# Performance work log

Measured on AMD Instinct MI355X. Metric: run time of the kernel, lower is better.

Reference implementation:

```python
import jax, jax.numpy as jnp
import numpy as np

FEAT_STRIDE = 16
SCALES = np.array([4.0, 8.0, 16.0])
RATIOS = np.array([0.5, 1.0, 2.0])
SAMPLE_DURATION = 16
TIME_DIM = [16]
NUM_ANCHORS = 9
BATCH = 32
FEAT_H = 64
FEAT_W = 64
POST_NMS_TOPN = 300


def _whctrs(a):
    w = a[2] - a[0] + 1.0
    h = a[3] - a[1] + 1.0
    return w, h, a[0] + 0.5 * (w - 1.0), a[1] + 0.5 * (h - 1.0)


def _mkanchors(ws, hs, xc, yc):
    ws = ws[:, None]
    hs = hs[:, None]
    return np.hstack([xc - 0.5 * (ws - 1.0), yc - 0.5 * (hs - 1.0),
                      xc + 0.5 * (ws - 1.0), yc + 0.5 * (hs - 1.0)])


def _generate_anchors(base_size=16, ratios=RATIOS, scales=SCALES):
    base = np.array([1.0, 1.0, base_size, base_size]) - 1.0
    w, h, xc, yc = _whctrs(base)
    size = w * h
    ws = np.round(np.sqrt(size / ratios))
    hs = np.round(ws * ratios)
    ratio_anchors = _mkanchors(ws, hs, xc, yc)
    out = []
    for i in range(ratio_anchors.shape[0]):
        w_i, h_i, x_i, y_i = _whctrs(ratio_anchors[i])
        out.append(_mkanchors(w_i * scales, h_i * scales, x_i, y_i))
    return np.vstack(out).astype(np.float32)  # (A, 4)


def _anchors_all(feat_h, feat_w):
    # shifted anchors over the feature grid, then temporal tiling per time_dim
    anchors = _generate_anchors()                                  # (A, 4)
    sx = np.arange(feat_w) * FEAT_STRIDE
    sy = np.arange(feat_h) * FEAT_STRIDE
    mx, my = np.meshgrid(sx, sy)
    shifts = np.stack([mx.ravel(), my.ravel(), mx.ravel(), my.ravel()], 1).astype(np.float32)
    anc = (anchors[None, :, :] + shifts[:, None, :]).reshape(-1, 4)  # (K*A, 4)
    sd = SAMPLE_DURATION
    parts = []
    for t in TIME_DIM:
        for j in range(sd - t + 1):
            full = np.zeros((sd, anc.shape[0], 4), np.float32)
            full[j:j + t] = anc
            parts.append(full.transpose(1, 0, 2))                   # (K*A, sd, 4)
    return np.concatenate(parts, 0).reshape(-1, sd * 4)             # (N, sd*4)


def setup_inputs() -> dict:
    key = jax.random.key(0)
    k1, k2 = jax.random.split(key)
    scores_in = jax.random.normal(k1, (BATCH, 2 * NUM_ANCHORS, FEAT_H, FEAT_W), jnp.float32)
    bbox_frame = jax.random.normal(k2, (BATCH, NUM_ANCHORS * SAMPLE_DURATION * 4, FEAT_H, FEAT_W), jnp.float32)
    im_info = jnp.tile(jnp.array([[FEAT_H * 16.0, FEAT_W * 16.0, 1.0]], jnp.float32), (BATCH, 1))
    return {"scores_in": scores_in, "bbox_frame": bbox_frame, "im_info": im_info,
            "post_nms_topN": POST_NMS_TOPN}


def reference(scores_in, bbox_frame, im_info, post_nms_topN):
    B, _, H, W = scores_in.shape
    sd4 = SAMPLE_DURATION * 4
    # fg scores -> (B, K*A) in (h, w, a) order matching the anchor layout
    scores = scores_in[:, NUM_ANCHORS:].transpose(0, 2, 3, 1).reshape(B, -1)
    deltas = bbox_frame.transpose(0, 2, 3, 1).reshape(B, -1, sd4)
    aa = jnp.asarray(_anchors_all(H, W))                             # (N, sd*4)
    # bbox_transform_inv with weights (1,1,1,1), per-frame groups of 4
    bb = aa.reshape(1, -1, SAMPLE_DURATION, 4)                       # (1, N, sd, 4)
    dd = deltas.reshape(B, -1, SAMPLE_DURATION, 4)                   # (B, N, sd, 4)
    w = bb[..., 2] - bb[..., 0] + 1.0
    h = bb[..., 3] - bb[..., 1] + 1.0
    cx = bb[..., 0] + 0.5 * w
    cy = bb[..., 1] + 0.5 * h
    pcx = dd[..., 0] * w + cx
    pcy = dd[..., 1] * h + cy
    pw = jnp.exp(dd[..., 2]) * w
    ph = jnp.exp(dd[..., 3]) * h
    # clip to image bounds per batch element
    xmax = im_info[:, 1, None, None] - 1.0                           # (B,1,1)
    ymax = im_info[:, 0, None, None] - 1.0
    x1 = jnp.clip(pcx - 0.5 * pw, 0.0, xmax)
    y1 = jnp.clip(pcy - 0.5 * ph, 0.0, ymax)
    x2 = jnp.clip(pcx + 0.5 * pw, 0.0, xmax)
    y2 = jnp.clip(pcy + 0.5 * ph, 0.0, ymax)
    proposals = jnp.stack([x1, y1, x2, y2], -1).reshape(B, -1, sd4)  # (B, N, sd*4)
    # per-image descending sort + top-k gather (the torch code applies no real NMS)
    top_scores, top_idx = jax.lax.top_k(scores, post_nms_topN)       # (B, topN)
    top_props = jnp.take_along_axis(proposals, top_idx[:, :, None], axis=1)
    batch_col = jnp.broadcast_to(jnp.arange(B, dtype=proposals.dtype)[:, None],
                                 (B, post_nms_topN))
    out = jnp.concatenate([batch_col[..., None], top_props, top_scores[..., None]], -1)
    return out  # (B, post_nms_topN, sd*4 + 2)
```

## Files before the change

kernel.cpp:

```cpp
#include <hip/hip_runtime.h>
#include <math.h>

#define BATCH    32
#define FH       64
#define FW       64
#define NA       9
#define NSCORE   (FH*FW*NA)
#define TOPN     300
#define SD       16
#define NTHREADS 1024
#define NBINS    16384
#define NWORDS   (NBINS/2)
#define CAND_CAP 1024

__constant__ float c_aw[NA] = {92.f,184.f,368.f,64.f,128.f,256.f,44.f,88.f,176.f};
__constant__ float c_ah[NA] = {48.f,96.f,192.f,64.f,128.f,256.f,88.f,176.f,352.f};

__device__ __forceinline__ unsigned f2key(float f) {
    unsigned u = __float_as_uint(f);
    return (u & 0x80000000u) ? ~u : (u | 0x80000000u);
}
__device__ __forceinline__ float key2f(unsigned k) {
    unsigned u = (k & 0x80000000u) ? (k & 0x7FFFFFFFu) : ~k;
    return __uint_as_float(u);
}

__global__ __launch_bounds__(NTHREADS)
void proposal_topk_kernel(const float* __restrict__ scores_in,
                          const float* __restrict__ bbox,
                          const float* __restrict__ im_info,
                          float* __restrict__ out)
{
    const int b   = blockIdx.x;
    const int tid = threadIdx.x;
    const float* sc = scores_in + ((size_t)b * 18 + NA) * (FH * FW);
    const float4* sc4 = (const float4*)sc;

    __shared__ unsigned hist[NWORDS];
    __shared__ unsigned pscan[NTHREADS];
    __shared__ unsigned long long cand[CAND_CAP];
    __shared__ unsigned s_t14, s_nsel;

    for (int i = tid; i < NWORDS; i += NTHREADS) hist[i] = 0u;
    __syncthreads();
    for (int j = tid; j < NSCORE / 4; j += NTHREADS) {
        float4 v = sc4[j];
        unsigned d0 = f2key(v.x) >> 18;
        unsigned d1 = f2key(v.y) >> 18;
        unsigned d2 = f2key(v.z) >> 18;
        unsigned d3 = f2key(v.w) >> 18;
        atomicAdd(&hist[d0 >> 1], 1u << ((d0 & 1u) << 4));
        atomicAdd(&hist[d1 >> 1], 1u << ((d1 & 1u) << 4));
        atomicAdd(&hist[d2 >> 1], 1u << ((d2 & 1u) << 4));
        atomicAdd(&hist[d3 >> 1], 1u << ((d3 & 1u) << 4));
    }
    __syncthreads();

    unsigned w[8];
    unsigned local = 0u;
    #pragma unroll
    for (int i = 0; i < 8; ++i) {
        w[i] = hist[tid * 8 + i];
        local += (w[i] & 0xFFFFu) + (w[i] >> 16);
    }
    pscan[tid] = local;
    __syncthreads();
    for (int off = 1; off < NTHREADS; off <<= 1) {
        unsigned v = pscan[tid];
        unsigned add = (tid + off < NTHREADS) ? pscan[tid + off] : 0u;
        __syncthreads();
        pscan[tid] = v + add;
        __syncthreads();
    }
    unsigned above_excl = (tid + 1 < NTHREADS) ? pscan[tid + 1] : 0u;
    if (above_excl < TOPN && above_excl + local >= TOPN) {
        unsigned cum = above_excl;
        for (int bi = 15; bi >= 0; --bi) {
            unsigned word = w[bi >> 1];
            unsigned c = (bi & 1) ? (word >> 16) : (word & 0xFFFFu);
            if (cum + c >= TOPN) { s_t14 = (unsigned)tid * 16u + (unsigned)bi; break; }
            cum += c;
        }
        s_nsel = 0u;
    }
    __syncthreads();
    const unsigned T14 = s_t14;

    for (int i = tid; i < CAND_CAP; i += NTHREADS) cand[i] = 0ull;
    __syncthreads();
    for (int j4 = tid; j4 < NSCORE / 4; j4 += NTHREADS) {
        float4 v = sc4[j4];
        #pragma unroll
        for (int c = 0; c < 4; ++c) {
            float f = (c == 0) ? v.x : (c == 1) ? v.y : (c == 2) ? v.z : v.w;
            unsigned k = f2key(f);
            if ((k >> 18) >= T14) {
                int j = j4 * 4 + c;
                unsigned a   = (unsigned)j >> 12;
                unsigned pos = (unsigned)j & 4095u;
                unsigned idx = pos * NA + a;
                unsigned p = atomicAdd(&s_nsel, 1u);
                if (p < CAND_CAP)
                    cand[p] = ((unsigned long long)k << 32) | (unsigned)(~idx);
            }
        }
    }
    __syncthreads();

    for (unsigned ksz = 2; ksz <= CAND_CAP; ksz <<= 1) {
        for (unsigned js = ksz >> 1; js > 0; js >>= 1) {
            unsigned i = (unsigned)tid, ixj = i ^ js;
            if (ixj > i) {
                bool desc = ((i & ksz) == 0);
                unsigned long long x = cand[i], y = cand[ixj];
                if (desc ? (x < y) : (x > y)) { cand[i] = y; cand[ixj] = x; }
            }
            __syncthreads();
        }
    }

    const float xmax = im_info[b * 3 + 1] - 1.0f;
    const float ymax = im_info[b * 3 + 0] - 1.0f;
    float* ob = out + (size_t)b * TOPN * 66;
    for (int item = tid; item < TOPN * SD; item += NTHREADS) {
        int r = item >> 4;
        int t = item & 15;
        unsigned long long e = cand[r];
        unsigned idx  = ~(unsigned)e;
        float  score  = key2f((unsigned)(e >> 32));
        unsigned a    = idx % 9u;
        unsigned pos  = idx / 9u;
        unsigned x    = pos & 63u;
        unsigned y    = pos >> 6;
        float w_  = c_aw[a], h_ = c_ah[a];
        float cx = 8.0f + 16.0f * (float)x;
        float cy = 8.0f + 16.0f * (float)y;
        const float* dp = bbox + (((size_t)b * 576 + (size_t)(a * 64 + t * 4)) << 12) + pos;
        float d0 = dp[0];
        float d1 = dp[4096];
        float d2 = dp[8192];
        float d3 = dp[12288];
        float pcx = d0 * w_ + cx;
        float pcy = d1 * h_ + cy;
        float pw  = expf(d2) * w_;
        float ph  = expf(d3) * h_;
        float x1 = fminf(fmaxf(pcx - 0.5f * pw, 0.0f), xmax);
        float y1 = fminf(fmaxf(pcy - 0.5f * ph, 0.0f), ymax);
        float x2 = fminf(fmaxf(pcx + 0.5f * pw, 0.0f), xmax);
        float y2 = fminf(fmaxf(pcy + 0.5f * ph, 0.0f), ymax);
        float* orow = ob + r * 66;
        orow[1 + t * 4 + 0] = x1;
        orow[1 + t * 4 + 1] = y1;
        orow[1 + t * 4 + 2] = x2;
        orow[1 + t * 4 + 3] = y2;
        if (t == 0) { orow[0] = (float)b; orow[65] = score; }
    }
}

extern "C" void kernel_launch(void* const* d_in, const int* in_sizes, int n_in,
                              void* d_out, int out_size, void* d_ws, size_t ws_size,
                              hipStream_t stream) {
    const float* scores_in = (const float*)d_in[0];
    const float* bbox      = (const float*)d_in[1];
    const float* im_info   = (const float*)d_in[2];
    float* out = (float*)d_out;
    proposal_topk_kernel<<<BATCH, NTHREADS, 0, stream>>>(scores_in, bbox, im_info, out);
}
```

Baseline: 409.6 us.

## Split top-k and decode into two kernels, rank-sort candidates, wave-shuffle scan

Splits the single per-batch kernel into a top-k kernel and a separate decode kernel launched across many more blocks, so the scattered bbox gathers and output writes spread over the whole GPU instead of 32 blocks. The top-k kernel keeps the scores in registers so the second global pass is gone, replaces the 1024-thread shared-memory scan with wave shuffles, and replaces the bitonic sort with a brute-force rank count over the candidates. It raises the candidate cap to 2048 and writes ranked results to workspace, at the cost of an extra launch, a global round-trip and quadratic rank work if many candidates fall past the threshold.

Result: faster. 372.2 us (-9.1%).

```diff
diff --git a/kernel.cpp b/kernel.cpp
--- a/kernel.cpp
+++ b/kernel.cpp
@@ -6,12 +6,15 @@
 #define FW       64
 #define NA       9
 #define NSCORE   (FH*FW*NA)
+#define NVEC     (NSCORE/4)
+#define VPT      (NVEC/1024)
 #define TOPN     300
 #define SD       16
 #define NTHREADS 1024
 #define NBINS    16384
 #define NWORDS   (NBINS/2)
-#define CAND_CAP 1024
+#define CAND_CAP 2048
+#define RB       19
 
 __constant__ float c_aw[NA] = {92.f,184.f,368.f,64.f,128.f,256.f,44.f,88.f,176.f};
 __constant__ float c_ah[NA] = {48.f,96.f,192.f,64.f,128.f,256.f,88.f,176.f,352.f};
@@ -26,29 +29,31 @@
 }
 
 __global__ __launch_bounds__(NTHREADS)
-void proposal_topk_kernel(const float* __restrict__ scores_in,
-                          const float* __restrict__ bbox,
-                          const float* __restrict__ im_info,
-                          float* __restrict__ out)
+void topk_kernel(const float* __restrict__ scores_in,
+                 unsigned long long* __restrict__ sel)
 {
-    const int b   = blockIdx.x;
-    const int tid = threadIdx.x;
-    const float* sc = scores_in + ((size_t)b * 18 + NA) * (FH * FW);
-    const float4* sc4 = (const float4*)sc;
+    const int b    = blockIdx.x;
+    const int tid  = threadIdx.x;
+    const int lane = tid & 63;
+    const int wv   = tid >> 6;
+    const float4* sc4 = (const float4*)(scores_in + ((size_t)b * 18 + NA) * (FH * FW));
 
     __shared__ unsigned hist[NWORDS];
-    __shared__ unsigned pscan[NTHREADS];
     __shared__ unsigned long long cand[CAND_CAP];
+    __shared__ unsigned wtot[16], wsuf[16];
     __shared__ unsigned s_t14, s_nsel;
 
     for (int i = tid; i < NWORDS; i += NTHREADS) hist[i] = 0u;
+    if (tid == 0) s_nsel = 0u;
     __syncthreads();
-    for (int j = tid; j < NSCORE / 4; j += NTHREADS) {
-        float4 v = sc4[j];
-        unsigned d0 = f2key(v.x) >> 18;
-        unsigned d1 = f2key(v.y) >> 18;
-        unsigned d2 = f2key(v.z) >> 18;
-        unsigned d3 = f2key(v.w) >> 18;
+    float4 v[VPT];
+    #pragma unroll
+    for (int k = 0; k < VPT; ++k) {
+        v[k] = sc4[tid + k * NTHREADS];
+        unsigned d0 = f2key(v[k].x) >> 18;
+        unsigned d1 = f2key(v[k].y) >> 18;
+        unsigned d2 = f2key(v[k].z) >> 18;
+        unsigned d3 = f2key(v[k].w) >> 18;
         atomicAdd(&hist[d0 >> 1], 1u << ((d0 & 1u) << 4));
         atomicAdd(&hist[d1 >> 1], 1u << ((d1 & 1u) << 4));
         atomicAdd(&hist[d2 >> 1], 1u << ((d2 & 1u) << 4));
@@ -63,16 +68,25 @@
         w[i] = hist[tid * 8 + i];
         local += (w[i] & 0xFFFFu) + (w[i] >> 16);
     }
-    pscan[tid] = local;
+    unsigned incl = local;
+    #pragma unroll
+    for (int off = 1; off < 64; off <<= 1) {
+        unsigned o = __shfl_down(incl, off);
+        if (lane + off < 64) incl += o;
+    }
+    if (lane == 0) wtot[wv] = incl;
     __syncthreads();
-    for (int off = 1; off < NTHREADS; off <<= 1) {
-        unsigned v = pscan[tid];
-        unsigned add = (tid + off < NTHREADS) ? pscan[tid + off] : 0u;
-        __syncthreads();
-        pscan[tid] = v + add;
-        __syncthreads();
+    if (tid < 16) {
+        unsigned x = wtot[tid];
+        #pragma unroll
+        for (int off = 1; off < 16; off <<= 1) {
+            unsigned o = __shfl_down(x, off, 16);
+            if ((tid & 15) + off < 16) x += o;
+        }
+        wsuf[tid] = x - wtot[tid];
     }
-    unsigned above_excl = (tid + 1 < NTHREADS) ? pscan[tid + 1] : 0u;
+    __syncthreads();
+    unsigned above_excl = wsuf[wv] + (incl - local);
     if (above_excl < TOPN && above_excl + local >= TOPN) {
         unsigned cum = above_excl;
         for (int bi = 15; bi >= 0; --bi) {
@@ -81,80 +95,82 @@
             if (cum + c >= TOPN) { s_t14 = (unsigned)tid * 16u + (unsigned)bi; break; }
             cum += c;
         }
-        s_nsel = 0u;
     }
     __syncthreads();
     const unsigned T14 = s_t14;
 
-    for (int i = tid; i < CAND_CAP; i += NTHREADS) cand[i] = 0ull;
-    __syncthreads();
-    for (int j4 = tid; j4 < NSCORE / 4; j4 += NTHREADS) {
-        float4 v = sc4[j4];
+    #pragma unroll
+    for (int k = 0; k < VPT; ++k) {
         #pragma unroll
         for (int c = 0; c < 4; ++c) {
-            float f = (c == 0) ? v.x : (c == 1) ? v.y : (c == 2) ? v.z : v.w;
-            unsigned k = f2key(f);
-            if ((k >> 18) >= T14) {
-                int j = j4 * 4 + c;
+            float f = (c == 0) ? v[k].x : (c == 1) ? v[k].y : (c == 2) ? v[k].z : v[k].w;
+            unsigned key = f2key(f);
+            if ((key >> 18) >= T14) {
+                int j = (tid + k * NTHREADS) * 4 + c;
                 unsigned a   = (unsigned)j >> 12;
                 unsigned pos = (unsigned)j & 4095u;
                 unsigned idx = pos * NA + a;
                 unsigned p = atomicAdd(&s_nsel, 1u);
                 if (p < CAND_CAP)
-                    cand[p] = ((unsigned long long)k << 32) | (unsigned)(~idx);
+                    cand[p] = ((unsigned long long)key << 32) | (unsigned)(~idx);
             }
         }
     }
     __syncthreads();
 
-    for (unsigned ksz = 2; ksz <= CAND_CAP; ksz <<= 1) {
-        for (unsigned js = ksz >> 1; js > 0; js >>= 1) {
-            unsigned i = (unsigned)tid, ixj = i ^ js;
-            if (ixj > i) {
-                bool desc = ((i & ksz) == 0);
-                unsigned long long x = cand[i], y = cand[ixj];
-                if (desc ? (x < y) : (x > y)) { cand[i] = y; cand[ixj] = x; }
-            }
-            __syncthreads();
-        }
+    unsigned n = s_nsel; if (n > CAND_CAP) n = CAND_CAP;
+    if (tid < (int)n) {
+        unsigned long long my = cand[tid];
+        unsigned rank = 0;
+        for (unsigned j = 0; j < n; ++j) rank += (cand[j] > my);
+        if (rank < TOPN) sel[(size_t)b * TOPN + rank] = my;
     }
+}
 
-    const float xmax = im_info[b * 3 + 1] - 1.0f;
-    const float ymax = im_info[b * 3 + 0] - 1.0f;
-    float* ob = out + (size_t)b * TOPN * 66;
-    for (int item = tid; item < TOPN * SD; item += NTHREADS) {
-        int r = item >> 4;
-        int t = item & 15;
-        unsigned long long e = cand[r];
-        unsigned idx  = ~(unsigned)e;
-        float  score  = key2f((unsigned)(e >> 32));
-        unsigned a    = idx % 9u;
-        unsigned pos  = idx / 9u;
-        unsigned x    = pos & 63u;
-        unsigned y    = pos >> 6;
-        float w_  = c_aw[a], h_ = c_ah[a];
-        float cx = 8.0f + 16.0f * (float)x;
-        float cy = 8.0f + 16.0f * (float)y;
-        const float* dp = bbox + (((size_t)b * 576 + (size_t)(a * 64 + t * 4)) << 12) + pos;
-        float d0 = dp[0];
-        float d1 = dp[4096];
-        float d2 = dp[8192];
-        float d3 = dp[12288];
-        float pcx = d0 * w_ + cx;
-        float pcy = d1 * h_ + cy;
-        float pw  = expf(d2) * w_;
-        float ph  = expf(d3) * h_;
-        float x1 = fminf(fmaxf(pcx - 0.5f * pw, 0.0f), xmax);
-        float y1 = fminf(fmaxf(pcy - 0.5f * ph, 0.0f), ymax);
-        float x2 = fminf(fmaxf(pcx + 0.5f * pw, 0.0f), xmax);
-        float y2 = fminf(fmaxf(pcy + 0.5f * ph, 0.0f), ymax);
-        float* orow = ob + r * 66;
-        orow[1 + t * 4 + 0] = x1;
-        orow[1 + t * 4 + 1] = y1;
-        orow[1 + t * 4 + 2] = x2;
-        orow[1 + t * 4 + 3] = y2;
-        if (t == 0) { orow[0] = (float)b; orow[65] = score; }
-    }
+__global__ __launch_bounds__(256)
+void decode_kernel(const float* __restrict__ bbox,
+                   const float* __restrict__ im_info,
+                   const unsigned long long* __restrict__ sel,
+                   float* __restrict__ out)
+{
+    const int b     = blockIdx.x / RB;
+    const int chunk = blockIdx.x % RB;
+    const int tid   = threadIdx.x;
+    const int r     = chunk * 16 + (tid >> 4);
+    const int t     = tid & 15;
+    if (r >= TOPN) return;
+
+    unsigned long long e = sel[(size_t)b * TOPN + r];
+    unsigned idx  = ~(unsigned)e;
+    float  score  = key2f((unsigned)(e >> 32));
+    unsigned a    = idx % 9u;
+    unsigned pos  = idx / 9u;
+    unsigned x    = pos & 63u;
+    unsigned y    = pos >> 6;
+    float w_ = c_aw[a], h_ = c_ah[a];
+    float cx = 8.0f + 16.0f * (float)x;
+    float cy = 8.0f + 16.0f * (float)y;
+    const float* dp = bbox + (((size_t)b * 576 + (size_t)(a * 64 + t * 4)) << 12) + pos;
+    float d0 = dp[0];
+    float d1 = dp[4096];
+    float d2 = dp[8192];
+    float d3 = dp[12288];
+    float xmax = im_info[b * 3 + 1] - 1.0f;
+    float ymax = im_info[b * 3 + 0] - 1.0f;
+    float pcx = d0 * w_ + cx;
+    float pcy = d1 * h_ + cy;
+    float pw  = expf(d2) * w_;
+    float ph  = expf(d3) * h_;
+    float x1 = fminf(fmaxf(pcx - 0.5f * pw, 0.0f), xmax);
+    float y1 = fminf(fmaxf(pcy - 0.5f * ph, 0.0f), ymax);
+    float x2 = fminf(fmaxf(pcx + 0.5f * pw, 0.0f), xmax);
+    float y2 = fminf(fmaxf(pcy + 0.5f * ph, 0.0f), ymax);
+    float* orow = out + ((size_t)b * TOPN + r) * 66;
+    orow[1 + t * 4 + 0] = x1;
+    orow[1 + t * 4 + 1] = y1;
+    orow[1 + t * 4 + 2] = x2;
+    orow[1 + t * 4 + 3] = y2;
+    if (t == 0) { orow[0] = (float)b; orow[65] = score; }
 }
 
 extern "C" void kernel_launch(void* const* d_in, const int* in_sizes, int n_in,
@@ -164,5 +180,8 @@
     const float* bbox      = (const float*)d_in[1];
     const float* im_info   = (const float*)d_in[2];
     float* out = (float*)d_out;
-    proposal_topk_kernel<<<BATCH, NTHREADS, 0, stream>>>(scores_in, bbox, im_info, out);
+    unsigned long long* sel = (unsigned long long*)d_ws;
+
+    topk_kernel<<<BATCH, NTHREADS, 0, stream>>>(scores_in, sel);
+    decode_kernel<<<BATCH * RB, 256, 0, stream>>>(bbox, im_info, sel, out);
 }
```
